# Kernel optimization log

Hardware: AMD Instinct MI355X
Metric: run time of the kernel (lower is better)

Reference implementation:

```python
import jax, jax.numpy as jnp
import numpy as np
from jax import lax

HEADS = 8  # ensembles * cells

def _conv(x, w, padding, groups):
    # NCHW grouped 2D convolution, stride 1
    return lax.conv_general_dilated(
        x, w, window_strides=(1, 1), padding=padding,
        feature_group_count=groups,
        dimension_numbers=('NCHW', 'OIHW', 'NCHW'))


def setup_inputs() -> dict:
    key = jax.random.key(0)
    ks = jax.random.split(key, 16)
    N, Cin, H, W = 8, 128, 36, 36
    C = 256                      # out_channels
    hc = C // HEADS              # head_channels = 32
    s = jnp.float32(0.05)        # weight scale to keep logits sane
    f32 = jnp.float32
    inp = {
        'x':  jax.random.normal(ks[0], (N, Cin, H, W), f32),
        'h0': jnp.zeros((N, C, H, W), f32),
        'c0': jnp.zeros((N, C, H, W), f32),
        'Wx': jax.random.normal(ks[1], (C, Cin, 1, 1), f32) * s,
        'Wq': jax.random.normal(ks[2], (C, 2 * hc, 3, 3), f32) * s,
        'Wk': jax.random.normal(ks[3], (C, 2 * hc, 3, 3), f32) * s,
        'Wv': jax.random.normal(ks[4], (C, 2 * hc, 3, 3), f32) * s,
        'Wi1': jax.random.normal(ks[5], (C, hc, 1, 1), f32) * s,
        'Wi2': jax.random.normal(ks[6], (C, 2 * hc, 3, 3), f32) * s,
        'bi': jnp.zeros((C,), f32),
        'Wf1': jax.random.normal(ks[7], (C, hc, 1, 1), f32) * s,
        'Wf2': jax.random.normal(ks[8], (C, 2 * hc, 3, 3), f32) * s,
        'bf': jnp.zeros((C,), f32),
        'Wg1': jax.random.normal(ks[9], (C, hc, 1, 1), f32) * s,
        'Wg2': jax.random.normal(ks[10], (C, 2 * hc, 3, 3), f32) * s,
        'bg': jnp.zeros((C,), f32),
        'Wo1': jax.random.normal(ks[11], (C, hc, 1, 1), f32) * s,
        'Wo2': jax.random.normal(ks[12], (C, 2 * hc, 3, 3), f32) * s,
        'bo': jnp.zeros((C,), f32),
        'tau': jnp.full((HEADS,), hc ** (-0.5), f32),
    }
    return inp


def reference(x, h0, c0, Wx, Wq, Wk, Wv, Wi1, Wi2, bi,
              Wf1, Wf2, bf, Wg1, Wg2, bg, Wo1, Wo2, bo, tau):
    N, _, H, W = x.shape
    G = tau.shape[0]
    # input projection (1x1 conv, no groups, no bias)
    xx = _conv(x, Wx, 'VALID', 1)          # [N, C, H, W]
    C = xx.shape[1]
    hc = C // G
    # stack x and h per head: [N, G, 2, hc, H, W] -> [N, 2C, H, W]
    xh = jnp.stack([xx.reshape(N, G, hc, H, W),
                    h0.reshape(N, G, hc, H, W)], axis=2)
    xh = xh.reshape(N, 2 * C, H, W)
    # q padded (SAME), k/v unpadded (VALID) -> mismatched spatial extents
    q = _conv(xh, Wq, 'SAME', G).reshape(N, G, hc, H * W)          # Q = H*W
    kc = _conv(xh, Wk, 'VALID', G)
    Dh, Dw = kc.shape[2], kc.shape[3]
    k = kc.reshape(N, G, hc, Dh * Dw)                              # D = (H-ks+1)*(W-ks+1)
    v = _conv(xh, Wv, 'VALID', G).reshape(N, G, hc, Dh * Dw)
    # attention: tau-scaled channel contraction, softmax over key positions
    logits = jnp.einsum('g,ngcq,ngcd->ngqd', tau, q, k)            # [N,G,Q,D]
    attn = jax.nn.softmax(logits, axis=3)
    a = jnp.einsum('ngcd,ngqd->ngcq', v, attn).reshape(N, C, H, W)

    def gate(W1, W2, b):
        # grouped 1x1 conv on a + grouped kxk SAME conv on xh + bias
        return (_conv(a, W1, 'VALID', G) + _conv(xh, W2, 'SAME', G)
                + b[None, :, None, None])

    i = jax.nn.sigmoid(gate(Wi1, Wi2, bi))
    f = jax.nn.sigmoid(gate(Wf1, Wf2, bf))
    g = jnp.tanh(gate(Wg1, Wg2, bg))
    o = jax.nn.sigmoid(gate(Wo1, Wo2, bo))
    c = f * c0 + i * g
    h = o * jnp.tanh(c)
    return h
```

## Files before the change

kernel.cpp:

```cpp
#include <hip/hip_runtime.h>
#include <math.h>

#define NN  8
#define CIN 128
#define HW  1296
#define CC  256
#define DDS 1156

typedef __attribute__((ext_vector_type(8))) short bvec8;
typedef __attribute__((ext_vector_type(4))) float fvec4;

__device__ __forceinline__ float sigmoidf_(float x) {
    return 1.f / (1.f + __expf(-x));
}
__device__ __forceinline__ float tanhf_(float x) {
    float xa = fminf(fmaxf(x, -15.f), 15.f);
    float e = __expf(2.f * xa);
    return (e - 1.f) / (e + 1.f);
}
__device__ __forceinline__ unsigned short f2bf(float f) {
    unsigned int u = __float_as_uint(f);
    u = (u + 0x7FFFu + ((u >> 16) & 1u)) >> 16;
    return (unsigned short)u;
}
__device__ __forceinline__ unsigned int cvtpk_bf16(float a, float b) {
    unsigned int r;
    asm("v_cvt_pk_bf16_f32 %0, %1, %2" : "=v"(r) : "v"(a), "v"(b));
    return r;
}
__device__ __forceinline__ float exp2a(float x) {
    float r;
    asm("v_exp_f32 %0, %1" : "=v"(r) : "v"(x));
    return r;
}

__global__ __launch_bounds__(256) void k_prep(
        const float* __restrict__ x, const float* __restrict__ h0,
        const float* __restrict__ Wx,
        const float* __restrict__ Wq, const float* __restrict__ Wk,
        const float* __restrict__ Wv, const float* __restrict__ tau,
        const float* __restrict__ Wi2, const float* __restrict__ Wf2,
        const float* __restrict__ Wg2, const float* __restrict__ Wo2,
        const float* __restrict__ Wi1, const float* __restrict__ Wf1,
        const float* __restrict__ Wg1, const float* __restrict__ Wo1,
        unsigned short* __restrict__ xb, unsigned short* __restrict__ h0b,
        unsigned short* __restrict__ apx, unsigned short* __restrict__ apq,
        unsigned short* __restrict__ apg2, unsigned short* __restrict__ apg1) {
    __shared__ float tr[10400];
    int bid = blockIdx.x;
    int tid = threadIdx.x;
    if (bid < 384) {
        int n = bid / 48, cb = bid % 48;
        const float* src = (cb < 16) ? x  + (size_t)(n * CIN + cb * 8) * HW
                                     : h0 + (size_t)(n * CC + (cb - 16) * 8) * HW;
        unsigned short* dst = (cb < 16) ? xb  + ((size_t)(n * 16 + cb) * HW) * 8
                                        : h0b + ((size_t)(n * 32 + (cb - 16)) * HW) * 8;
        #pragma unroll
        for (int c = 0; c < 8; ++c)
            for (int p4 = tid; p4 < 324; p4 += 256) {
                float4 v = ((const float4*)(src + (size_t)c * HW))[p4];
                *(float4*)&tr[c * 1300 + p4 * 4] = v;
            }
        __syncthreads();
        for (int p = tid; p < 1296; p += 256) {
            union { unsigned short us[8]; bvec8 v; } pk;
            #pragma unroll
            for (int c = 0; c < 8; ++c) pk.us[c] = f2bf(tr[c * 1300 + p]);
            *(bvec8*)(dst + (size_t)p * 8) = pk.v;
        }
        return;
    }
    int t = (bid - 384) * 256 + tid;
    union { unsigned short us[8]; bvec8 v; } pk;
    if (t < 55296) {
        int u = t;
        int lane = u & 63;
        int t2 = u >> 6;
        int mf = t2 % 6, t3 = t2 / 6;
        int s = t3 % 18, g = t3 / 18;
        int kyx = s >> 1, icb = s & 1;
        int ky = kyx / 3, kx = kyx % 3;
        int m = mf * 16 + (lane & 15);
        int conv = m >> 5, cl = m & 31, co = g * 32 + cl;
        int ic0 = icb * 32 + (lane >> 4) * 8;
        const float* W = (conv == 0) ? Wq : (conv == 1 ? Wk : Wv);
        float scale = (conv == 0) ? tau[g] * 1.4426950408889634f : 1.f;
        #pragma unroll
        for (int j = 0; j < 8; ++j)
            pk.us[j] = f2bf(W[((co * 64 + ic0 + j) * 3 + ky) * 3 + kx] * scale);
        *(bvec8*)(apq + (size_t)u * 8) = pk.v;
    } else if (t < 59392) {
        int u = t - 55296;
        int lane = u & 63;
        int t2 = u >> 6;
        int mf = t2 % 16, s = t2 / 16;
        int co = mf * 16 + (lane & 15);
        int k0 = s * 32 + (lane >> 4) * 8;
        #pragma unroll
        for (int j = 0; j < 8; ++j)
            pk.us[j] = f2bf(Wx[co * CIN + k0 + j]);
        *(bvec8*)(apx + (size_t)u * 8) = pk.v;
    } else if (t < 133120) {
        int u = t - 59392;
        int lane = u & 63;
        int t2 = u >> 6;
        int mf = t2 % 8, t3 = t2 / 8;
        int s = t3 % 18, g = t3 / 18;
        int kyx = s >> 1, icb = s & 1;
        int ky = kyx / 3, kx = kyx % 3;
        int m = mf * 16 + (lane & 15);
        int gate = m >> 5, cl = m & 31, co = g * 32 + cl;
        int ic0 = icb * 32 + (lane >> 4) * 8;
        const float* W = (gate == 0) ? Wi2 : (gate == 1 ? Wf2 : (gate == 2 ? Wg2 : Wo2));
        #pragma unroll
        for (int j = 0; j < 8; ++j)
            pk.us[j] = f2bf(W[((co * 64 + ic0 + j) * 3 + ky) * 3 + kx]);
        *(bvec8*)(apg2 + (size_t)u * 8) = pk.v;
    } else if (t < 137216) {
        int u = t - 133120;
        int lane = u & 63;
        int t2 = u >> 6;
        int mf = t2 % 8, g = t2 / 8;
        int m = mf * 16 + (lane & 15);
        int gate = m >> 5, cl = m & 31, co = g * 32 + cl;
        int k0 = (lane >> 4) * 8;
        const float* W = (gate == 0) ? Wi1 : (gate == 1 ? Wf1 : (gate == 2 ? Wg1 : Wo1));
        #pragma unroll
        for (int j = 0; j < 8; ++j)
            pk.us[j] = f2bf(W[co * 32 + k0 + j]);
        *(bvec8*)(apg1 + (size_t)u * 8) = pk.v;
    }
}

__global__ __launch_bounds__(256) void k_xx_mfma(
        const unsigned short* __restrict__ xb, const unsigned short* __restrict__ apx,
        unsigned short* __restrict__ xxb) {
    int bid = blockIdx.x;
    int n = bid / 27, pc = bid % 27;
    int tid = threadIdx.x;
    int w = tid >> 6, lane = tid & 63;
    int ln = lane & 15, kgrp = lane >> 4;
    const bvec8* A = (const bvec8*)apx;
    bvec8 af[4][4];
    #pragma unroll
    for (int s = 0; s < 4; ++s)
        #pragma unroll
        for (int i = 0; i < 4; ++i)
            af[s][i] = A[(s * 16 + w * 4 + i) * 64 + lane];
    fvec4 acc[4][3];
    #pragma unroll
    for (int i = 0; i < 4; ++i)
        #pragma unroll
        for (int jn = 0; jn < 3; ++jn)
            acc[i][jn] = fvec4{0.f, 0.f, 0.f, 0.f};
    #pragma unroll
    for (int s = 0; s < 4; ++s) {
        #pragma unroll
        for (int jn = 0; jn < 3; ++jn) {
            int p = pc * 48 + jn * 16 + ln;
            bvec8 bfr = *(const bvec8*)(xb + ((size_t)(n * 16 + s * 4 + kgrp) * HW + p) * 8);
            #pragma unroll
            for (int i = 0; i < 4; ++i)
                acc[i][jn] = __builtin_amdgcn_mfma_f32_16x16x32_bf16(af[s][i], bfr, acc[i][jn], 0, 0, 0);
        }
    }
    #pragma unroll
    for (int i = 0; i < 4; ++i) {
        int co0 = (w * 4 + i) * 16 + kgrp * 4;
        int icb = co0 >> 3, sub = co0 & 7;
        #pragma unroll
        for (int jn = 0; jn < 3; ++jn) {
            int p = pc * 48 + jn * 16 + ln;
            union { unsigned short us[4]; unsigned long long u; } pk;
            #pragma unroll
            for (int r = 0; r < 4; ++r) pk.us[r] = f2bf(acc[i][jn][r]);
            *(unsigned long long*)(xxb + ((size_t)(n * 32 + icb) * HW + p) * 8 + sub) = pk.u;
        }
    }
}

__global__ __launch_bounds__(384) void k_qkv_mfma(
        const unsigned short* __restrict__ xxb, const unsigned short* __restrict__ h0b,
        const unsigned short* __restrict__ apq,
        unsigned short* __restrict__ qT, unsigned short* __restrict__ kT,
        unsigned short* __restrict__ vB) {
    int bid = blockIdx.x;
    int n = bid / 72, rem = bid % 72;
    int g = rem / 9, yt = rem % 9;
    __shared__ bvec8 sm[1824];
    int tid = threadIdx.x;
    for (int u = tid; u < 1824; u += 384) {
        int col = u % 38; int t2 = u / 38;
        int icb = t2 % 8; int rr = t2 / 8;
        int y = yt * 4 - 1 + rr, cx = col - 1;
        bvec8 val = {0, 0, 0, 0, 0, 0, 0, 0};
        if (y >= 0 && y < 36 && cx >= 0 && cx < 36) {
            const unsigned short* src = (icb < 4)
                ? (xxb + ((size_t)(n * 32 + g * 4 + icb) * HW) * 8)
                : (h0b + ((size_t)(n * 32 + g * 4 + icb - 4) * HW) * 8);
            val = *(const bvec8*)(src + (size_t)(y * 36 + cx) * 8);
        }
        int s = rr * 38 + col;
        sm[s * 8 + (icb ^ (s & 7))] = val;
    }
    __syncthreads();
    int lane = tid & 63, w = tid >> 6;
    int mg = w % 3, nh = w / 3;
    int kgrp = lane >> 4;
    int nf0 = nh * 4;
    int sb[5], pl[5];
    #pragma unroll
    for (int jn = 0; jn < 5; ++jn) {
        int p = (nf0 + jn) * 16 + (lane & 15);
        pl[jn] = p;
        sb[jn] = (p / 36) * 38 + (p % 36);
    }
    fvec4 acc[2][5];
    #pragma unroll
    for (int i = 0; i < 2; ++i)
        #pragma unroll
        for (int jn = 0; jn < 5; ++jn)
            acc[i][jn] = fvec4{0.f, 0.f, 0.f, 0.f};
    const bvec8* ap = (const bvec8*)apq + (size_t)g * 6912 + mg * 128 + lane;
    for (int s = 0; s < 18; ++s) {
        int kyx = s >> 1, icb = s & 1;
        int ky = kyx / 3, kx = kyx % 3;
        bvec8 a0 = ap[0], a1 = ap[64];
        ap += 384;
        int soff = ky * 38 + kx;
        int ib = icb * 4 + kgrp;
        #pragma unroll
        for (int jn = 0; jn < 5; ++jn) {
            int slot = sb[jn] + soff;
            bvec8 bfr = sm[slot * 8 + (ib ^ (slot & 7))];
            acc[0][jn] = __builtin_amdgcn_mfma_f32_16x16x32_bf16(a0, bfr, acc[0][jn], 0, 0, 0);
            acc[1][jn] = __builtin_amdgcn_mfma_f32_16x16x32_bf16(a1, bfr, acc[1][jn], 0, 0, 0);
        }
    }
    int ngb = n * 8 + g;
    unsigned short* qTg = qT + (size_t)ngb * 41472;
    unsigned short* kTg = kT + (size_t)ngb * 36992;
    unsigned short* vBg = vB + (size_t)ngb * 37120;
    #pragma unroll
    for (int i = 0; i < 2; ++i) {
        int mf = mg * 2 + i;
        int m0 = mf * 16 + kgrp * 4;
        int conv = m0 >> 5, c0 = m0 & 31;
        #pragma unroll
        for (int jn = 0; jn < 5; ++jn) {
            int gp = yt * 144 + pl[jn];
            int py = gp / 36, px = gp % 36;
            if (conv == 0) {
                union { unsigned short us[4]; unsigned long long u; } pk;
                #pragma unroll
                for (int r = 0; r < 4; ++r) pk.us[r] = f2bf(acc[i][jn][r]);
                *(unsigned long long*)(qTg + (size_t)gp * 32 + c0) = pk.u;
            } else if (py >= 1 && py <= 34 && px >= 1 && px <= 34) {
                int dpix = (py - 1) * 34 + (px - 1);
                if (conv == 1) {
                    union { unsigned short us[4]; unsigned long long u; } pk;
                    #pragma unroll
                    for (int r = 0; r < 4; ++r) pk.us[r] = f2bf(acc[i][jn][r]);
                    *(unsigned long long*)(kTg + (size_t)dpix * 32 + c0) = pk.u;
                } else {
                    #pragma unroll
                    for (int r = 0; r < 4; ++r)
                        vBg[(size_t)(c0 + r) * 1160 + dpix] = f2bf(acc[i][jn][r]);
                }
            }
        }
    }
}

__global__ __launch_bounds__(256) void k_attn_mfma(
        const unsigned short* __restrict__ qT, const unsigned short* __restrict__ kT,
        const unsigned short* __restrict__ vB, unsigned short* __restrict__ ab) {
    int bid = blockIdx.x;
    int ng = bid / 21, bt = bid % 21;
    int tid = threadIdx.x;
    int w = tid >> 6, l = tid & 63;
    int qblk = bt * 4 + w;
    bool qvalid = qblk < 81;
    int qb = qvalid ? qblk : 80;
    int ln = l & 15, g = l >> 4;
    __shared__ unsigned short sP[4][640];
    const unsigned short* qTg = qT + (size_t)ng * 41472;
    const unsigned short* kTg = kT + (size_t)ng * 36992;
    const unsigned short* vBg = vB + (size_t)ng * 37120;
    bvec8 qf = *(const bvec8*)(qTg + (size_t)(qb * 16 + ln) * 32 + g * 8);
    const unsigned short* kp = kTg + ln * 32 + g * 8;
    const unsigned short* vp = vBg + (size_t)ln * 1160 + g * 8;
    unsigned short* sw0 = &sP[w][ln * 40 + g * 4];
    unsigned short* sw1 = &sP[w][ln * 40 + 16 + g * 4];
    const unsigned short* sr = &sP[w][ln * 40 + g * 8];
    fvec4 acc0 = {0.f, 0.f, 0.f, 0.f}, acc1 = {0.f, 0.f, 0.f, 0.f};
    fvec4 zero = {0.f, 0.f, 0.f, 0.f};
    float lp = 0.f;
    bvec8 ka0 = *(const bvec8*)(kp);
    bvec8 ka1 = *(const bvec8*)(kp + 512);
    bvec8 va0 = *(const bvec8*)(vp);
    bvec8 va1 = *(const bvec8*)(vp + 18560);
    #pragma unroll 2
    for (int t = 0; t < 36; ++t) {
        int tn = (t < 35) ? t + 1 : 35;
        bvec8 nk0 = *(const bvec8*)(kp + tn * 1024);
        bvec8 nk1 = *(const bvec8*)(kp + tn * 1024 + 512);
        bvec8 nv0 = *(const bvec8*)(vp + tn * 32);
        bvec8 nv1 = *(const bvec8*)(vp + tn * 32 + 18560);
        fvec4 s0 = __builtin_amdgcn_mfma_f32_16x16x32_bf16(ka0, qf, zero, 0, 0, 0);
        fvec4 s1 = __builtin_amdgcn_mfma_f32_16x16x32_bf16(ka1, qf, zero, 0, 0, 0);
        float p[8];
        #pragma unroll
        for (int r = 0; r < 4; ++r) {
            p[r]     = exp2a(s0[r]);
            p[4 + r] = exp2a(s1[r]);
        }
        lp += ((p[0] + p[1]) + (p[2] + p[3])) + ((p[4] + p[5]) + (p[6] + p[7]));
        union { unsigned int ui[2]; unsigned long long u; } w0, w1;
        w0.ui[0] = cvtpk_bf16(p[0], p[1]);
        w0.ui[1] = cvtpk_bf16(p[2], p[3]);
        w1.ui[0] = cvtpk_bf16(p[4], p[5]);
        w1.ui[1] = cvtpk_bf16(p[6], p[7]);
        *(unsigned long long*)sw0 = w0.u;
        *(unsigned long long*)sw1 = w1.u;
        bvec8 pB = *(const bvec8*)sr;
        acc0 = __builtin_amdgcn_mfma_f32_16x16x32_bf16(va0, pB, acc0, 0, 0, 0);
        acc1 = __builtin_amdgcn_mfma_f32_16x16x32_bf16(va1, pB, acc1, 0, 0, 0);
        ka0 = nk0; ka1 = nk1; va0 = nv0; va1 = nv1;
    }
    {
        bvec8 tk = *(const bvec8*)(kTg + (size_t)min(1152 + ln, 1155) * 32 + g * 8);
        fvec4 s0 = __builtin_amdgcn_mfma_f32_16x16x32_bf16(tk, qf, zero, 0, 0, 0);
        float p[4];
        #pragma unroll
        for (int r = 0; r < 4; ++r)
            p[r] = (g == 0) ? exp2a(s0[r]) : 0.f;
        lp += (p[0] + p[1]) + (p[2] + p[3]);
        union { unsigned int ui[2]; unsigned long long u; } w0;
        w0.ui[0] = cvtpk_bf16(p[0], p[1]);
        w0.ui[1] = cvtpk_bf16(p[2], p[3]);
        *(unsigned long long*)sw0 = w0.u;
        *(unsigned long long*)sw1 = 0ull;
        bvec8 pB = *(const bvec8*)sr;
        bvec8 tv0 = *(const bvec8*)(vp + 36 * 32);
        bvec8 tv1 = *(const bvec8*)(vp + 36 * 32 + 18560);
        acc0 = __builtin_amdgcn_mfma_f32_16x16x32_bf16(tv0, pB, acc0, 0, 0, 0);
        acc1 = __builtin_amdgcn_mfma_f32_16x16x32_bf16(tv1, pB, acc1, 0, 0, 0);
    }
    float lt = lp;
    lt += __shfl_xor(lt, 16, 64);
    lt += __shfl_xor(lt, 32, 64);
    float inv = 1.f / lt;
    if (qvalid) {
        int qpos = qblk * 16 + ln;
        unsigned short* ag = ab + (size_t)ng * 41472;
        int sub = (g & 1) * 4;
        union { unsigned short us[4]; unsigned long long u; } pk0, pk1;
        #pragma unroll
        for (int r = 0; r < 4; ++r) {
            pk0.us[r] = f2bf(acc0[r] * inv);
            pk1.us[r] = f2bf(acc1[r] * inv);
        }
        *(unsigned long long*)(ag + ((size_t)(g >> 1) * HW + qpos) * 8 + sub)       = pk0.u;
        *(unsigned long long*)(ag + ((size_t)(2 + (g >> 1)) * HW + qpos) * 8 + sub) = pk1.u;
    }
}

__global__ __launch_bounds__(256) void k_gates_mfma(
        const unsigned short* __restrict__ xxb, const unsigned short* __restrict__ h0b,
        const float* __restrict__ c0, const unsigned short* __restrict__ ab,
        const unsigned short* __restrict__ apg2, const unsigned short* __restrict__ apg1,
        const float* __restrict__ bi, const float* __restrict__ bf_,
        const float* __restrict__ bg, const float* __restrict__ bo,
        float* __restrict__ out) {
    int bid = blockIdx.x;
    int n = bid / 72, rem = bid % 72;
    int g = rem / 9, yt = rem % 9;
    __shared__ bvec8 smx[1824];
    __shared__ bvec8 sma[576];
    int tid = threadIdx.x;
    for (int u = tid; u < 1824; u += 256) {
        int col = u % 38; int t2 = u / 38;
        int icb = t2 % 8; int rr = t2 / 8;
        int y = yt * 4 - 1 + rr, cx = col - 1;
        bvec8 val = {0, 0, 0, 0, 0, 0, 0, 0};
        if (y >= 0 && y < 36 && cx >= 0 && cx < 36) {
            const unsigned short* src = (icb < 4)
                ? (xxb + ((size_t)(n * 32 + g * 4 + icb) * HW) * 8)
                : (h0b + ((size_t)(n * 32 + g * 4 + icb - 4) * HW) * 8);
            val = *(const bvec8*)(src + (size_t)(y * 36 + cx) * 8);
        }
        int s = rr * 38 + col;
        smx[s * 8 + (icb ^ (s & 7))] = val;
    }
    int ngb = n * 8 + g;
    for (int u = tid; u < 576; u += 256) {
        int p = u % 144, cb = u / 144;
        int gp = yt * 144 + p;
        bvec8 val = *(const bvec8*)(ab + ((size_t)(ngb * 4 + cb) * HW + gp) * 8);
        sma[p * 4 + (cb ^ (p & 3))] = val;
    }
    __syncthreads();
    int lane = tid & 63, w = tid >> 6;
    int b = w & 1, nh = w >> 1;
    int kgrp = lane >> 4, nf0 = nh * 4;
    int sb[5], pl[5];
    #pragma unroll
    for (int jn = 0; jn < 5; ++jn) {
        int p = (nf0 + jn) * 16 + (lane & 15);
        pl[jn] = p;
        sb[jn] = (p / 36) * 38 + (p % 36);
    }
    fvec4 acc[4][5];
    #pragma unroll
    for (int i = 0; i < 4; ++i)
        #pragma unroll
        for (int jn = 0; jn < 5; ++jn)
            acc[i][jn] = fvec4{0.f, 0.f, 0.f, 0.f};
    const bvec8* ap = (const bvec8*)apg2 + ((size_t)g * 144 + b) * 64 + lane;
    for (int s = 0; s < 18; ++s) {
        int kyx = s >> 1, icb = s & 1;
        int ky = kyx / 3, kx = kyx % 3;
        bvec8 a0 = ap[0], a1 = ap[128], a2 = ap[256], a3 = ap[384];
        ap += 512;
        int soff = ky * 38 + kx;
        int ib = icb * 4 + kgrp;
        #pragma unroll
        for (int jn = 0; jn < 5; ++jn) {
            int slot = sb[jn] + soff;
            bvec8 bfr = smx[slot * 8 + (ib ^ (slot & 7))];
            acc[0][jn] = __builtin_amdgcn_mfma_f32_16x16x32_bf16(a0, bfr, acc[0][jn], 0, 0, 0);
            acc[1][jn] = __builtin_amdgcn_mfma_f32_16x16x32_bf16(a1, bfr, acc[1][jn], 0, 0, 0);
            acc[2][jn] = __builtin_amdgcn_mfma_f32_16x16x32_bf16(a2, bfr, acc[2][jn], 0, 0, 0);
            acc[3][jn] = __builtin_amdgcn_mfma_f32_16x16x32_bf16(a3, bfr, acc[3][jn], 0, 0, 0);
        }
    }
    {
        const bvec8* ap1 = (const bvec8*)apg1 + ((size_t)g * 8 + b) * 64 + lane;
        bvec8 a0 = ap1[0], a1 = ap1[128], a2 = ap1[256], a3 = ap1[384];
        #pragma unroll
        for (int jn = 0; jn < 5; ++jn) {
            int p = pl[jn];
            bvec8 bfr = sma[p * 4 + (kgrp ^ (p & 3))];
            acc[0][jn] = __builtin_amdgcn_mfma_f32_16x16x32_bf16(a0, bfr, acc[0][jn], 0, 0, 0);
            acc[1][jn] = __builtin_amdgcn_mfma_f32_16x16x32_bf16(a1, bfr, acc[1][jn], 0, 0, 0);
            acc[2][jn] = __builtin_amdgcn_mfma_f32_16x16x32_bf16(a2, bfr, acc[2][jn], 0, 0, 0);
            acc[3][jn] = __builtin_amdgcn_mfma_f32_16x16x32_bf16(a3, bfr, acc[3][jn], 0, 0, 0);
        }
    }
    #pragma unroll
    for (int jn = 0; jn < 5; ++jn) {
        int gp = yt * 144 + pl[jn];
        #pragma unroll
        for (int r = 0; r < 4; ++r) {
            int cl = b * 16 + kgrp * 4 + r;
            int co = g * 32 + cl;
            float ip   = acc[0][jn][r] + bi[co];
            float fp   = acc[1][jn][r] + bf_[co];
            float gpre = acc[2][jn][r] + bg[co];
            float op   = acc[3][jn][r] + bo[co];
            float iv = sigmoidf_(ip), fv = sigmoidf_(fp);
            float gv = tanhf_(gpre), ov = sigmoidf_(op);
            float cv = fmaf(fv, c0[(size_t)(n * CC + co) * HW + gp], iv * gv);
            out[(size_t)(n * CC + co) * HW + gp] = ov * tanhf_(cv);
        }
    }
}

extern "C" void kernel_launch(void* const* d_in, const int* in_sizes, int n_in,
                              void* d_out, int out_size, void* d_ws, size_t ws_size,
                              hipStream_t stream) {
    const float* x   = (const float*)d_in[0];
    const float* h0  = (const float*)d_in[1];
    const float* c0  = (const float*)d_in[2];
    const float* Wx  = (const float*)d_in[3];
    const float* Wq  = (const float*)d_in[4];
    const float* Wk  = (const float*)d_in[5];
    const float* Wv  = (const float*)d_in[6];
    const float* Wi1 = (const float*)d_in[7];
    const float* Wi2 = (const float*)d_in[8];
    const float* bi  = (const float*)d_in[9];
    const float* Wf1 = (const float*)d_in[10];
    const float* Wf2 = (const float*)d_in[11];
    const float* bf  = (const float*)d_in[12];
    const float* Wg1 = (const float*)d_in[13];
    const float* Wg2 = (const float*)d_in[14];
    const float* bg  = (const float*)d_in[15];
    const float* Wo1 = (const float*)d_in[16];
    const float* Wo2 = (const float*)d_in[17];
    const float* bo  = (const float*)d_in[18];
    const float* tau = (const float*)d_in[19];

    unsigned short* ws  = (unsigned short*)d_ws;
    unsigned short* xb   = ws;
    unsigned short* h0b  = xb   + 1327104;
    unsigned short* xxb  = h0b  + 2654208;
    unsigned short* ab   = xxb  + 2654208;
    unsigned short* qT   = ab   + 2654208;
    unsigned short* kT   = qT   + 2654208;
    unsigned short* vB   = kT   + 2367488;
    unsigned short* apx  = vB   + 2375744;
    unsigned short* apq  = apx  + 32768;
    unsigned short* apg2 = apq  + 442368;
    unsigned short* apg1 = apg2 + 589824;
    float* out = (float*)d_out;

    hipLaunchKernelGGL(k_prep, dim3(920), dim3(256), 0, stream,
                       x, h0, Wx, Wq, Wk, Wv, tau,
                       Wi2, Wf2, Wg2, Wo2, Wi1, Wf1, Wg1, Wo1,
                       xb, h0b, apx, apq, apg2, apg1);
    hipLaunchKernelGGL(k_xx_mfma,   dim3(216),  dim3(256), 0, stream, xb, apx, xxb);
    hipLaunchKernelGGL(k_qkv_mfma,  dim3(576),  dim3(384), 0, stream, xxb, h0b, apq, qT, kT, vB);
    hipLaunchKernelGGL(k_attn_mfma, dim3(1344), dim3(256), 0, stream, qT, kT, vB, ab);
    hipLaunchKernelGGL(k_gates_mfma,dim3(576),  dim3(256), 0, stream, xxb, h0b, c0, ab,
                       apg2, apg1, bi, bf, bg, bo, out);
}
```

Measured before the change: 127.4 us.

## Permute V layout so softmax probabilities feed MFMA directly from registers

The QKV kernel now writes V with a permuted key order inside each 32-key tile, so the layout matches the register layout of the QK^T MFMA output. The attention kernel can then pack the exponentiated scores straight into the B operand of the PV MFMA. This drops the per-iteration LDS write, the LDS read and the shared buffer. The V buffer row stride grows slightly to hold padded tiles, and the QKV epilogue gains a few index computations.

```diff
diff --git a/kernel.cpp b/kernel.cpp
--- a/kernel.cpp
+++ b/kernel.cpp
@@ -183,7 +183,7 @@
         const unsigned short* __restrict__ xxb, const unsigned short* __restrict__ h0b,
         const unsigned short* __restrict__ apq,
         unsigned short* __restrict__ qT, unsigned short* __restrict__ kT,
-        unsigned short* __restrict__ vB) {
+        unsigned short* __restrict__ vS) {
     int bid = blockIdx.x;
     int n = bid / 72, rem = bid % 72;
     int g = rem / 9, yt = rem % 9;
@@ -240,7 +240,7 @@
     int ngb = n * 8 + g;
     unsigned short* qTg = qT + (size_t)ngb * 41472;
     unsigned short* kTg = kT + (size_t)ngb * 36992;
-    unsigned short* vBg = vB + (size_t)ngb * 37120;
+    unsigned short* vSg = vS + (size_t)ngb * 37888;
     #pragma unroll
     for (int i = 0; i < 2; ++i) {
         int mf = mg * 2 + i;
@@ -263,9 +263,12 @@
                     for (int r = 0; r < 4; ++r) pk.us[r] = f2bf(acc[i][jn][r]);
                     *(unsigned long long*)(kTg + (size_t)dpix * 32 + c0) = pk.u;
                 } else {
+                    int tt = dpix >> 5, kk = dpix & 31;
+                    int slot = ((kk & 15) >> 2) * 8 + ((kk >> 4) << 2) + (kk & 3);
+                    int idx = tt * 32 + slot;
                     #pragma unroll
                     for (int r = 0; r < 4; ++r)
-                        vBg[(size_t)(c0 + r) * 1160 + dpix] = f2bf(acc[i][jn][r]);
+                        vSg[(size_t)(c0 + r) * 1184 + idx] = f2bf(acc[i][jn][r]);
                 }
             }
         }
@@ -274,7 +277,7 @@
 
 __global__ __launch_bounds__(256) void k_attn_mfma(
         const unsigned short* __restrict__ qT, const unsigned short* __restrict__ kT,
-        const unsigned short* __restrict__ vB, unsigned short* __restrict__ ab) {
+        const unsigned short* __restrict__ vS, unsigned short* __restrict__ ab) {
     int bid = blockIdx.x;
     int ng = bid / 21, bt = bid % 21;
     int tid = threadIdx.x;
@@ -283,30 +286,26 @@
     bool qvalid = qblk < 81;
     int qb = qvalid ? qblk : 80;
     int ln = l & 15, g = l >> 4;
-    __shared__ unsigned short sP[4][640];
     const unsigned short* qTg = qT + (size_t)ng * 41472;
     const unsigned short* kTg = kT + (size_t)ng * 36992;
-    const unsigned short* vBg = vB + (size_t)ng * 37120;
+    const unsigned short* vSg = vS + (size_t)ng * 37888;
     bvec8 qf = *(const bvec8*)(qTg + (size_t)(qb * 16 + ln) * 32 + g * 8);
     const unsigned short* kp = kTg + ln * 32 + g * 8;
-    const unsigned short* vp = vBg + (size_t)ln * 1160 + g * 8;
-    unsigned short* sw0 = &sP[w][ln * 40 + g * 4];
-    unsigned short* sw1 = &sP[w][ln * 40 + 16 + g * 4];
-    const unsigned short* sr = &sP[w][ln * 40 + g * 8];
+    const unsigned short* vp = vSg + (size_t)ln * 1184 + g * 8;
     fvec4 acc0 = {0.f, 0.f, 0.f, 0.f}, acc1 = {0.f, 0.f, 0.f, 0.f};
     fvec4 zero = {0.f, 0.f, 0.f, 0.f};
     float lp = 0.f;
     bvec8 ka0 = *(const bvec8*)(kp);
     bvec8 ka1 = *(const bvec8*)(kp + 512);
     bvec8 va0 = *(const bvec8*)(vp);
-    bvec8 va1 = *(const bvec8*)(vp + 18560);
+    bvec8 va1 = *(const bvec8*)(vp + 18944);
     #pragma unroll 2
     for (int t = 0; t < 36; ++t) {
         int tn = (t < 35) ? t + 1 : 35;
         bvec8 nk0 = *(const bvec8*)(kp + tn * 1024);
         bvec8 nk1 = *(const bvec8*)(kp + tn * 1024 + 512);
         bvec8 nv0 = *(const bvec8*)(vp + tn * 32);
-        bvec8 nv1 = *(const bvec8*)(vp + tn * 32 + 18560);
+        bvec8 nv1 = *(const bvec8*)(vp + tn * 32 + 18944);
         fvec4 s0 = __builtin_amdgcn_mfma_f32_16x16x32_bf16(ka0, qf, zero, 0, 0, 0);
         fvec4 s1 = __builtin_amdgcn_mfma_f32_16x16x32_bf16(ka1, qf, zero, 0, 0, 0);
         float p[8];
@@ -316,16 +315,13 @@
             p[4 + r] = exp2a(s1[r]);
         }
         lp += ((p[0] + p[1]) + (p[2] + p[3])) + ((p[4] + p[5]) + (p[6] + p[7]));
-        union { unsigned int ui[2]; unsigned long long u; } w0, w1;
-        w0.ui[0] = cvtpk_bf16(p[0], p[1]);
-        w0.ui[1] = cvtpk_bf16(p[2], p[3]);
-        w1.ui[0] = cvtpk_bf16(p[4], p[5]);
-        w1.ui[1] = cvtpk_bf16(p[6], p[7]);
-        *(unsigned long long*)sw0 = w0.u;
-        *(unsigned long long*)sw1 = w1.u;
-        bvec8 pB = *(const bvec8*)sr;
-        acc0 = __builtin_amdgcn_mfma_f32_16x16x32_bf16(va0, pB, acc0, 0, 0, 0);
-        acc1 = __builtin_amdgcn_mfma_f32_16x16x32_bf16(va1, pB, acc1, 0, 0, 0);
+        union { unsigned int ui[4]; bvec8 v; } pB;
+        pB.ui[0] = cvtpk_bf16(p[0], p[1]);
+        pB.ui[1] = cvtpk_bf16(p[2], p[3]);
+        pB.ui[2] = cvtpk_bf16(p[4], p[5]);
+        pB.ui[3] = cvtpk_bf16(p[6], p[7]);
+        acc0 = __builtin_amdgcn_mfma_f32_16x16x32_bf16(va0, pB.v, acc0, 0, 0, 0);
+        acc1 = __builtin_amdgcn_mfma_f32_16x16x32_bf16(va1, pB.v, acc1, 0, 0, 0);
         ka0 = nk0; ka1 = nk1; va0 = nv0; va1 = nv1;
     }
     {
@@ -336,16 +332,15 @@
         for (int r = 0; r < 4; ++r)
             p[r] = (g == 0) ? exp2a(s0[r]) : 0.f;
         lp += (p[0] + p[1]) + (p[2] + p[3]);
-        union { unsigned int ui[2]; unsigned long long u; } w0;
-        w0.ui[0] = cvtpk_bf16(p[0], p[1]);
-        w0.ui[1] = cvtpk_bf16(p[2], p[3]);
-        *(unsigned long long*)sw0 = w0.u;
-        *(unsigned long long*)sw1 = 0ull;
-        bvec8 pB = *(const bvec8*)sr;
+        union { unsigned int ui[4]; bvec8 v; } pB;
+        pB.ui[0] = cvtpk_bf16(p[0], p[1]);
+        pB.ui[1] = cvtpk_bf16(p[2], p[3]);
+        pB.ui[2] = 0u;
+        pB.ui[3] = 0u;
         bvec8 tv0 = *(const bvec8*)(vp + 36 * 32);
-        bvec8 tv1 = *(const bvec8*)(vp + 36 * 32 + 18560);
-        acc0 = __builtin_amdgcn_mfma_f32_16x16x32_bf16(tv0, pB, acc0, 0, 0, 0);
-        acc1 = __builtin_amdgcn_mfma_f32_16x16x32_bf16(tv1, pB, acc1, 0, 0, 0);
+        bvec8 tv1 = *(const bvec8*)(vp + 36 * 32 + 18944);
+        acc0 = __builtin_amdgcn_mfma_f32_16x16x32_bf16(tv0, pB.v, acc0, 0, 0, 0);
+        acc1 = __builtin_amdgcn_mfma_f32_16x16x32_bf16(tv1, pB.v, acc1, 0, 0, 0);
     }
     float lt = lp;
     lt += __shfl_xor(lt, 16, 64);
@@ -498,8 +493,8 @@
     unsigned short* ab   = xxb  + 2654208;
     unsigned short* qT   = ab   + 2654208;
     unsigned short* kT   = qT   + 2654208;
-    unsigned short* vB   = kT   + 2367488;
-    unsigned short* apx  = vB   + 2375744;
+    unsigned short* vS   = kT   + 2367488;
+    unsigned short* apx  = vS   + 2424832;
     unsigned short* apq  = apx  + 32768;
     unsigned short* apg2 = apq  + 442368;
     unsigned short* apg1 = apg2 + 589824;
@@ -510,8 +505,8 @@
                        Wi2, Wf2, Wg2, Wo2, Wi1, Wf1, Wg1, Wo1,
                        xb, h0b, apx, apq, apg2, apg1);
     hipLaunchKernelGGL(k_xx_mfma,   dim3(216),  dim3(256), 0, stream, xb, apx, xxb);
-    hipLaunchKernelGGL(k_qkv_mfma,  dim3(576),  dim3(384), 0, stream, xxb, h0b, apq, qT, kT, vB);
-    hipLaunchKernelGGL(k_attn_mfma, dim3(1344), dim3(256), 0, stream, qT, kT, vB, ab);
+    hipLaunchKernelGGL(k_qkv_mfma,  dim3(576),  dim3(384), 0, stream, xxb, h0b, apq, qT, kT, vS);
+    hipLaunchKernelGGL(k_attn_mfma, dim3(1344), dim3(256), 0, stream, qT, kT, vS, ab);
     hipLaunchKernelGGL(k_gates_mfma,dim3(576),  dim3(256), 0, stream, xxb, h0b, c0, ab,
                        apg2, apg1, bi, bf, bg, bo, out);
 }
```

After: 134.8 us. 1.06x slower.
